# Kernel tuning notes

Hardware: AMD Instinct MI355X
Metric: run time of the kernel (lower is better)

## Reference

```python
import jax, jax.numpy as jnp
import numpy as np


def setup_inputs() -> dict:
    key = jax.random.key(0)
    ks = jax.random.split(key, 5)
    B, C, H, W = 8, 256, 64, 64
    Ck = C // 8  # 32, reduced channel dim
    return {
        "x": jax.random.normal(ks[0], (B, C, H, W), dtype=jnp.float32),
        "wf": jax.random.normal(ks[1], (Ck, C), dtype=jnp.float32) * 0.05,
        "wg": jax.random.normal(ks[2], (Ck, C), dtype=jnp.float32) * 0.05,
        "wh": jax.random.normal(ks[3], (Ck, C), dtype=jnp.float32) * 0.05,
        "wv": jax.random.normal(ks[4], (C, Ck), dtype=jnp.float32) * 0.05,
        "gamma": jnp.zeros((1,), dtype=jnp.float32),
    }


def reference(x, wf, wg, wh, wv, gamma):
    B, C, H, W = x.shape
    N = H * W
    xf = x.reshape(B, C, N)  # flatten spatial tokens
    # 1x1 convs == channel matmuls
    f = jnp.einsum('oc,bcn->bon', wf, xf)  # [B, Ck, N]
    g = jnp.einsum('oc,bcn->bon', wg, xf)  # [B, Ck, N]
    h = jnp.einsum('oc,bcn->bon', wh, xf)  # [B, Ck, N]
    # s = f^T @ g -> [B, N, N]; softmax over last axis (dim 2 in torch)
    s = jnp.einsum('bcn,bcm->bnm', f, g)
    beta = jax.nn.softmax(s, axis=2)
    # v = h @ beta  (note: beta NOT transposed, faithful to original)
    v = jnp.einsum('bcn,bnm->bcm', h, beta)  # [B, Ck, N]
    o = jnp.einsum('oc,bcm->bom', wv, v).reshape(B, C, H, W)
    return gamma * o + x
```

## Files before the change

kernel.cpp:

```cpp
#include <hip/hip_runtime.h>
#include <hip/hip_bf16.h>

#define BB 8
#define CC 256
#define CK 32
#define NN 4096

typedef short bf16x8 __attribute__((ext_vector_type(8)));
typedef float f32x4 __attribute__((ext_vector_type(4)));

#define MFMA(a, b, c) __builtin_amdgcn_mfma_f32_16x16x32_bf16((a), (b), (c), 0, 0, 0)

#define GLOAD16(gsrc, ldst) __builtin_amdgcn_global_load_lds( \
    (const __attribute__((address_space(1))) void*)(gsrc), \
    (__attribute__((address_space(3))) void*)(ldst), 16, 0, 0)

#define OBASE(b) ((size_t)(b) * 1048576)
#define OFF_F  0
#define OFF_G  65536
#define OFF_HT 131072
#define OFF_LE 196608
#define OFF_V0 200704
#define OFF_WB 786432
#define VSTRIDE 131072

#define SHIFT 24.0f

static __device__ __forceinline__ unsigned pack_trunc(float lo, float hi) {
  unsigned ulo = __builtin_bit_cast(unsigned, lo);
  unsigned uhi = __builtin_bit_cast(unsigned, hi);
  return (uhi & 0xFFFF0000u) | (ulo >> 16);
}
static __device__ __forceinline__ unsigned pack_rne(float lo, float hi) {
  unsigned ulo = __builtin_bit_cast(unsigned, lo);
  unsigned uhi = __builtin_bit_cast(unsigned, hi);
  ulo += 0x7FFFu + ((ulo >> 16) & 1u);
  uhi += 0x7FFFu + ((uhi >> 16) & 1u);
  return (uhi & 0xFFFF0000u) | (ulo >> 16);
}
static __device__ __forceinline__ unsigned short rne16(float v) {
  unsigned u = __builtin_bit_cast(unsigned, v);
  u += 0x7FFFu + ((u >> 16) & 1u);
  return (unsigned short)(u >> 16);
}

__global__ __launch_bounds__(256) void wcvt_kernel(
    const float* __restrict__ wf, const float* __restrict__ wg,
    const float* __restrict__ wh, float* __restrict__ sc)
{
  int w = blockIdx.x;
  int tid = threadIdx.x;
  const float* src = (w == 0) ? wf : ((w == 1) ? wg : wh);
  unsigned short* wb = (unsigned short*)(sc + OFF_WB) + w * 8192;
  for (int e = tid; e < 8192; e += 256) wb[e] = rne16(src[e]);
}

__global__ __launch_bounds__(256) void proj_kernel(
    const float* __restrict__ x, float* __restrict__ sc)
{
  __shared__ float t[64][69];
  __shared__ unsigned short tb[64][264];

  int tid = threadIdx.x, blk = blockIdx.x;
  int b = blk >> 6, n0 = (blk & 63) << 6;

  #pragma unroll 1
  for (int ct = 0; ct < 4; ++ct) {
    int c0 = ct << 6;
    const float* xb = x + ((size_t)b * CC + c0) * NN + n0;
    int ci0 = tid >> 4, j = (tid & 15) << 2;
    #pragma unroll
    for (int p = 0; p < 4; ++p) {
      int ci = p * 16 + ci0;
      float4 v = *(const float4*)&xb[(size_t)ci * NN + j];
      t[ci][j] = v.x; t[ci][j + 1] = v.y; t[ci][j + 2] = v.z; t[ci][j + 3] = v.w;
    }
    __syncthreads();
    int ni = tid >> 2, cq = (tid & 3) << 4;
    #pragma unroll
    for (int e = 0; e < 16; ++e)
      tb[ni][c0 + cq + e] = rne16(t[cq + e][ni]);
    __syncthreads();
  }

  int w = tid >> 6, lane = tid & 63, q = lane >> 4, c = lane & 15;
  int nb = n0 + (w << 4);
  const char* wB = (const char*)(sc + OFF_WB);
  const unsigned short* tbrow = &tb[(w << 4) + c][0];

  const f32x4 z4 = {0.f, 0.f, 0.f, 0.f};
  f32x4 fa0 = z4, fa1 = z4, ga0 = z4, ga1 = z4, ha0 = z4, ha1 = z4;

  #pragma unroll
  for (int kc = 0; kc < 8; ++kc) {
    int koe = kc * 32 + q * 8;
    int ko = kc * 64 + q * 16;
    bf16x8 xa = *(const bf16x8*)(tbrow + koe);
    bf16x8 w0 = *(const bf16x8*)(wB + (size_t)c * 512 + ko);
    bf16x8 w1 = *(const bf16x8*)(wB + (size_t)(16 + c) * 512 + ko);
    bf16x8 w2 = *(const bf16x8*)(wB + 16384 + (size_t)c * 512 + ko);
    bf16x8 w3 = *(const bf16x8*)(wB + 16384 + (size_t)(16 + c) * 512 + ko);
    bf16x8 w4 = *(const bf16x8*)(wB + 32768 + (size_t)c * 512 + ko);
    bf16x8 w5 = *(const bf16x8*)(wB + 32768 + (size_t)(16 + c) * 512 + ko);
    fa0 = MFMA(xa, w0, fa0);  fa1 = MFMA(xa, w1, fa1);
    ga0 = MFMA(xa, w2, ga0);  ga1 = MFMA(xa, w3, ga1);
    ha0 = MFMA(w4, xa, ha0);  ha1 = MFMA(w5, xa, ha1);
  }

  unsigned short* fD = (unsigned short*)(sc + OBASE(b) + OFF_F);
  unsigned short* gD = (unsigned short*)(sc + OBASE(b) + OFF_G);
  unsigned short* hD = (unsigned short*)(sc + OBASE(b) + OFF_HT);
  #pragma unroll
  for (int r = 0; r < 4; ++r) {
    int n = nb + q * 4 + r;
    fD[(size_t)n * 32 + c]      = rne16(fa0[r]);
    fD[(size_t)n * 32 + 16 + c] = rne16(fa1[r]);
    gD[(size_t)n * 32 + c]      = rne16(ga0[r]);
    gD[(size_t)n * 32 + 16 + c] = rne16(ga1[r]);
    hD[(size_t)(q * 4 + r) * NN + nb + c]        = rne16(ha0[r]);
    hD[(size_t)(16 + q * 4 + r) * NN + nb + c]   = rne16(ha1[r]);
  }
}

__global__ __launch_bounds__(256) void passb_kernel(float* __restrict__ sc)
{
  __shared__ float Zsh[2][16][4];
  int tid = threadIdx.x, blk = blockIdx.x;
  int b = blk >> 7, nb0 = (blk & 127) << 5;
  int w = tid >> 6, lane = tid & 63, q = lane >> 4, c = lane & 15;

  const char* fb = (const char*)(sc + OBASE(b) + OFF_F);
  const char* gb = (const char*)(sc + OBASE(b) + OFF_G);

  bf16x8 fa0 = *(const bf16x8*)(fb + (size_t)(nb0 + c) * 64 + q * 16);
  bf16x8 fa1 = *(const bf16x8*)(fb + (size_t)(nb0 + 16 + c) * 64 + q * 16);
  const f32x4 z4 = {0.f, 0.f, 0.f, 0.f};
  float za[2][4] = {{0.f,0.f,0.f,0.f},{0.f,0.f,0.f,0.f}};

  int mt0 = w << 10;
  bf16x8 g0 = *(const bf16x8*)(gb + (size_t)(mt0 + 0  + c) * 64 + q * 16);
  bf16x8 g1 = *(const bf16x8*)(gb + (size_t)(mt0 + 16 + c) * 64 + q * 16);
  bf16x8 g2 = *(const bf16x8*)(gb + (size_t)(mt0 + 32 + c) * 64 + q * 16);
  bf16x8 g3 = *(const bf16x8*)(gb + (size_t)(mt0 + 48 + c) * 64 + q * 16);

  for (int mt = mt0; mt < mt0 + 1024; mt += 64) {
    int mtn = (mt + 64 < mt0 + 1024) ? mt + 64 : mt0;
    bf16x8 n0 = *(const bf16x8*)(gb + (size_t)(mtn + 0  + c) * 64 + q * 16);
    bf16x8 n1 = *(const bf16x8*)(gb + (size_t)(mtn + 16 + c) * 64 + q * 16);
    bf16x8 n2 = *(const bf16x8*)(gb + (size_t)(mtn + 32 + c) * 64 + q * 16);
    bf16x8 n3 = *(const bf16x8*)(gb + (size_t)(mtn + 48 + c) * 64 + q * 16);
    f32x4 s;
    #define BSTEP(gk) \
      s = MFMA(fa0, gk, z4); \
      za[0][0] += __expf(s[0] - SHIFT); za[0][1] += __expf(s[1] - SHIFT); \
      za[0][2] += __expf(s[2] - SHIFT); za[0][3] += __expf(s[3] - SHIFT); \
      s = MFMA(fa1, gk, z4); \
      za[1][0] += __expf(s[0] - SHIFT); za[1][1] += __expf(s[1] - SHIFT); \
      za[1][2] += __expf(s[2] - SHIFT); za[1][3] += __expf(s[3] - SHIFT);
    BSTEP(g0) BSTEP(g1) BSTEP(g2) BSTEP(g3)
    #undef BSTEP
    g0 = n0; g1 = n1; g2 = n2; g3 = n3;
  }
  #pragma unroll
  for (int d = 1; d < 16; d <<= 1) {
    #pragma unroll
    for (int i = 0; i < 2; ++i)
      #pragma unroll
      for (int r = 0; r < 4; ++r) za[i][r] += __shfl_xor(za[i][r], d);
  }
  if (c == 0) {
    #pragma unroll
    for (int i = 0; i < 2; ++i)
      #pragma unroll
      for (int r = 0; r < 4; ++r) Zsh[i][q * 4 + r][w] = za[i][r];
  }
  __syncthreads();
  if (tid < 32) {
    int ns2 = tid >> 4, row = tid & 15;
    float Z = Zsh[ns2][row][0] + Zsh[ns2][row][1]
            + Zsh[ns2][row][2] + Zsh[ns2][row][3];
    sc[OBASE(b) + OFF_LE + nb0 + ns2 * 16 + row] = SHIFT + __logf(Z);
  }
}

__global__ __launch_bounds__(256, 4) void passc_kernel(float* __restrict__ sc)
{
  __shared__ unsigned Pt[128 * 32];
  __shared__ float Lsh[1024];
  __shared__ unsigned fsh[2][1024];
  __shared__ unsigned hsh[2][1024];

  int tid = threadIdx.x, blk = blockIdx.x;
  int b = blk >> 7, rest = blk & 127;
  int ns = rest & 3, mblk = rest >> 2;
  int m0 = mblk << 7;
  int nbase = ns << 10;
  int w = tid >> 6, lane = tid & 63, q = lane >> 4, c = lane & 15;
  int hc = tid >> 3, hslot = (tid & 7) ^ (hc & 7);

  const char* fb = (const char*)(sc + OBASE(b) + OFF_F);
  const char* gb = (const char*)(sc + OBASE(b) + OFF_G);
  const char* hb = (const char*)(sc + OBASE(b) + OFF_HT);
  const float* LE = sc + OBASE(b) + OFF_LE;

  for (int i = tid; i < 1024; i += 256) Lsh[i] = LE[nbase + i];

  bf16x8 gB0 = *(const bf16x8*)(gb + (size_t)(m0 + w * 16 + c) * 64 + q * 16);
  bf16x8 gB1 = *(const bf16x8*)(gb + (size_t)(m0 + 64 + w * 16 + c) * 64 + q * 16);

  GLOAD16(fb + (size_t)nbase * 64 + tid * 16, (char*)&fsh[0][0] + tid * 16);
  GLOAD16(hb + (size_t)hc * 8192 + (size_t)nbase * 2 + hslot * 16,
          (char*)&hsh[0][0] + tid * 16);
  __syncthreads();

  const f32x4 z4 = {0.f, 0.f, 0.f, 0.f};
  f32x4 v00 = z4, v01 = z4, v10 = z4, v11 = z4;

  unsigned sw = (unsigned)(c & 7) << 4;
  char* Pt0 = (char*)Pt + (size_t)(w * 16 + c) * 128;
  char* Pt1 = (char*)Pt + (size_t)(64 + w * 16 + c) * 128;

  int buf = 0;
  for (int nt = 0; nt < 1024; nt += 64) {
    if (nt + 64 < 1024) {
      GLOAD16(fb + (size_t)(nbase + nt + 64) * 64 + tid * 16,
              (char*)&fsh[buf ^ 1][0] + tid * 16);
      GLOAD16(hb + (size_t)hc * 8192 + (size_t)(nbase + nt + 64) * 2 + hslot * 16,
              (char*)&hsh[buf ^ 1][0] + tid * 16);
    }
    const char* fS = (const char*)&fsh[buf][0];
    const char* hS = (const char*)&hsh[buf][0];

    bf16x8 f0 = *(const bf16x8*)(fS + (0 * 16 + c) * 64 + q * 16);
    bf16x8 f1 = *(const bf16x8*)(fS + (1 * 16 + c) * 64 + q * 16);
    bf16x8 f2 = *(const bf16x8*)(fS + (2 * 16 + c) * 64 + q * 16);
    bf16x8 f3 = *(const bf16x8*)(fS + (3 * 16 + c) * 64 + q * 16);
    f32x4 sA0 = MFMA(f0, gB0, z4), sB0 = MFMA(f0, gB1, z4);
    f32x4 sA1 = MFMA(f1, gB0, z4), sB1 = MFMA(f1, gB1, z4);
    f32x4 sA2 = MFMA(f2, gB0, z4), sB2 = MFMA(f2, gB1, z4);
    f32x4 sA3 = MFMA(f3, gB0, z4), sB3 = MFMA(f3, gB1, z4);

    #pragma unroll
    for (int sub = 0; sub < 4; ++sub) {
      f32x4 sA = (sub == 0) ? sA0 : (sub == 1) ? sA1 : (sub == 2) ? sA2 : sA3;
      f32x4 sB = (sub == 0) ? sB0 : (sub == 1) ? sB1 : (sub == 2) ? sB2 : sB3;
      const f32x4 Lt = *(const f32x4*)&Lsh[nt + sub * 16 + q * 4];
      uint2 pkA, pkB;
      pkA.x = pack_trunc(__expf(sA[0] - Lt[0]), __expf(sA[1] - Lt[1]));
      pkA.y = pack_trunc(__expf(sA[2] - Lt[2]), __expf(sA[3] - Lt[3]));
      pkB.x = pack_trunc(__expf(sB[0] - Lt[0]), __expf(sB[1] - Lt[1]));
      pkB.y = pack_trunc(__expf(sB[2] - Lt[2]), __expf(sB[3] - Lt[3]));
      unsigned off = ((unsigned)(sub * 32 + q * 8)) ^ sw;
      *(uint2*)(Pt0 + off) = pkA;
      *(uint2*)(Pt1 + off) = pkB;
    }

    #pragma unroll
    for (int ks = 0; ks < 2; ++ks) {
      unsigned off = ((unsigned)(ks * 64 + q * 16)) ^ sw;
      bf16x8 pb0 = *(const bf16x8*)(Pt0 + off);
      bf16x8 pb1 = *(const bf16x8*)(Pt1 + off);
      bf16x8 h0 = *(const bf16x8*)(hS + c * 128 + off);
      bf16x8 h1 = *(const bf16x8*)(hS + (16 + c) * 128 + off);
      v00 = MFMA(h0, pb0, v00);
      v10 = MFMA(h1, pb0, v10);
      v01 = MFMA(h0, pb1, v01);
      v11 = MFMA(h1, pb1, v11);
    }
    __syncthreads();
    buf ^= 1;
  }

  float* V = sc + OBASE(b) + OFF_V0 + (size_t)ns * VSTRIDE;
  {
    int mA = m0 + w * 16 + c, mB = m0 + 64 + w * 16 + c;
    size_t bA = (size_t)(mA & 31) * 4096 + (size_t)(mA >> 5) * 32;
    size_t bB = (size_t)(mB & 31) * 4096 + (size_t)(mB >> 5) * 32;
    *(f32x4*)&V[bA + q * 4]      = v00;
    *(f32x4*)&V[bA + 16 + q * 4] = v10;
    *(f32x4*)&V[bB + q * 4]      = v01;
    *(f32x4*)&V[bB + 16 + q * 4] = v11;
  }
}

__global__ __launch_bounds__(256) void epi_kernel(
    float* out, const float* __restrict__ x,
    const float* __restrict__ wv, const float* __restrict__ gamma)
{
  int tid = threadIdx.x, blk = blockIdx.x;
  int b = blk >> 7;
  int m0 = (blk & 127) << 5;
  int w = tid >> 6, lane = tid & 63, q = lane >> 4, c = lane & 15;
  int co0 = w << 6;

  const float* V0 = out + OBASE(b) + OFF_V0;

  bf16x8 Bf[2];
  #pragma unroll
  for (int mt = 0; mt < 2; ++mt) {
    int ml = mt * 16 + c;
    size_t base = (size_t)ml * 4096 + (size_t)(m0 >> 5) * 32 + q * 8;
    float4 a0 = {0,0,0,0}, a1 = {0,0,0,0};
    #pragma unroll
    for (int i = 0; i < 4; ++i) {
      const float* Vi = V0 + (size_t)i * VSTRIDE;
      float4 p0 = *(const float4*)&Vi[base];
      float4 p1 = *(const float4*)&Vi[base + 4];
      a0.x += p0.x; a0.y += p0.y; a0.z += p0.z; a0.w += p0.w;
      a1.x += p1.x; a1.y += p1.y; a1.z += p1.z; a1.w += p1.w;
    }
    unsigned u0 = pack_rne(a0.x, a0.y);
    unsigned u1 = pack_rne(a0.z, a0.w);
    unsigned u2 = pack_rne(a1.x, a1.y);
    unsigned u3 = pack_rne(a1.z, a1.w);
    Bf[mt] = __builtin_bit_cast(bf16x8, make_uint4(u0, u1, u2, u3));
  }
  bf16x8 Af[4];
  #pragma unroll
  for (int ci = 0; ci < 4; ++ci) {
    const float* wr = wv + (size_t)(co0 + ci * 16 + c) * 32 + q * 8;
    float4 a0 = *(const float4*)wr;
    float4 a1 = *(const float4*)(wr + 4);
    unsigned u0 = pack_rne(a0.x, a0.y);
    unsigned u1 = pack_rne(a0.z, a0.w);
    unsigned u2 = pack_rne(a1.x, a1.y);
    unsigned u3 = pack_rne(a1.z, a1.w);
    Af[ci] = __builtin_bit_cast(bf16x8, make_uint4(u0, u1, u2, u3));
  }
  __syncthreads();

  const f32x4 z4 = {0.f, 0.f, 0.f, 0.f};
  const float g0 = gamma[0];
  #pragma unroll
  for (int ci = 0; ci < 4; ++ci) {
    #pragma unroll
    for (int mt = 0; mt < 2; ++mt) {
      f32x4 acc = MFMA(Af[ci], Bf[mt], z4);
      #pragma unroll
      for (int r = 0; r < 4; ++r) {
        int co = co0 + ci * 16 + q * 4 + r;
        size_t idx = ((size_t)b * CC + co) * NN + m0 + mt * 16 + c;
        out[idx] = g0 * acc[r] + x[idx];
      }
    }
  }
}

extern "C" void kernel_launch(void* const* d_in, const int* in_sizes, int n_in,
                              void* d_out, int out_size, void* d_ws, size_t ws_size,
                              hipStream_t stream) {
  const float* x     = (const float*)d_in[0];
  const float* wf    = (const float*)d_in[1];
  const float* wg    = (const float*)d_in[2];
  const float* wh    = (const float*)d_in[3];
  const float* wv    = (const float*)d_in[4];
  const float* gamma = (const float*)d_in[5];
  float* out = (float*)d_out;

  wcvt_kernel <<<3,    256, 0, stream>>>(wf, wg, wh, out);
  proj_kernel <<<512,  256, 0, stream>>>(x, out);
  passb_kernel<<<1024, 256, 0, stream>>>(out);
  passc_kernel<<<1024, 256, 0, stream>>>(out);
  epi_kernel  <<<1024, 256, 0, stream>>>(out, x, wv, gamma);
}
```

Baseline: 108.8 us.

## Fold softmax normalizer into h, use exp2 with constant shift, vectorize epilogue

Passb now computes the reciprocal of each row's softmax sum and scales the corresponding h columns in place, instead of storing a per-row log-sum. Passc can then use a fixed shift with exp2 and a fused multiply-add rather than loading and subtracting per-row normalizers, which removes the shared-memory normalizer load. The epilogue stages MFMA results through shared memory so that x is read and out written as coalesced float4 rows. The trade-off is an extra h rounding step, an in-place read-modify-write in passb, and the LDS transpose in the epilogue.

```diff
diff --git a/kernel.cpp b/kernel.cpp
--- a/kernel.cpp
+++ b/kernel.cpp
@@ -19,12 +19,13 @@
 #define OFF_F  0
 #define OFF_G  65536
 #define OFF_HT 131072
-#define OFF_LE 196608
 #define OFF_V0 200704
 #define OFF_WB 786432
 #define VSTRIDE 131072
 
 #define SHIFT 24.0f
+#define L2E 1.44269504089f
+#define S2  34.6246810188f
 
 static __device__ __forceinline__ unsigned pack_trunc(float lo, float hi) {
   unsigned ulo = __builtin_bit_cast(unsigned, lo);
@@ -43,6 +44,7 @@
   u += 0x7FFFu + ((u >> 16) & 1u);
   return (unsigned short)(u >> 16);
 }
+static __device__ __forceinline__ float fexp2(float y) { return __builtin_exp2f(y); }
 
 __global__ __launch_bounds__(256) void wcvt_kernel(
     const float* __restrict__ wf, const float* __restrict__ wg,
@@ -125,6 +127,7 @@
 __global__ __launch_bounds__(256) void passb_kernel(float* __restrict__ sc)
 {
   __shared__ float Zsh[2][16][4];
+  __shared__ float Rsh[32];
   int tid = threadIdx.x, blk = blockIdx.x;
   int b = blk >> 7, nb0 = (blk & 127) << 5;
   int w = tid >> 6, lane = tid & 63, q = lane >> 4, c = lane & 15;
@@ -179,14 +182,28 @@
     int ns2 = tid >> 4, row = tid & 15;
     float Z = Zsh[ns2][row][0] + Zsh[ns2][row][1]
             + Zsh[ns2][row][2] + Zsh[ns2][row][3];
-    sc[OBASE(b) + OFF_LE + nb0 + ns2 * 16 + row] = SHIFT + __logf(Z);
+    Rsh[ns2 * 16 + row] = 1.0f / Z;
+  }
+  __syncthreads();
+  {
+    int cidx = tid >> 3, jj = (tid & 7) << 2;
+    unsigned short* hp = (unsigned short*)(sc + OBASE(b) + OFF_HT)
+                       + (size_t)cidx * NN + nb0 + jj;
+    uint2 hv = *(const uint2*)hp;
+    float h0 = __builtin_bit_cast(float, hv.x << 16)          * Rsh[jj + 0];
+    float h1 = __builtin_bit_cast(float, hv.x & 0xFFFF0000u)  * Rsh[jj + 1];
+    float h2 = __builtin_bit_cast(float, hv.y << 16)          * Rsh[jj + 2];
+    float h3 = __builtin_bit_cast(float, hv.y & 0xFFFF0000u)  * Rsh[jj + 3];
+    uint2 ov;
+    ov.x = pack_rne(h0, h1);
+    ov.y = pack_rne(h2, h3);
+    *(uint2*)hp = ov;
   }
 }
 
 __global__ __launch_bounds__(256, 4) void passc_kernel(float* __restrict__ sc)
 {
-  __shared__ unsigned Pt[128 * 32];
-  __shared__ float Lsh[1024];
+  __shared__ unsigned Pt[128 * 32 + 1024];
   __shared__ unsigned fsh[2][1024];
   __shared__ unsigned hsh[2][1024];
 
@@ -201,9 +218,6 @@
   const char* fb = (const char*)(sc + OBASE(b) + OFF_F);
   const char* gb = (const char*)(sc + OBASE(b) + OFF_G);
   const char* hb = (const char*)(sc + OBASE(b) + OFF_HT);
-  const float* LE = sc + OBASE(b) + OFF_LE;
-
-  for (int i = tid; i < 1024; i += 256) Lsh[i] = LE[nbase + i];
 
   bf16x8 gB0 = *(const bf16x8*)(gb + (size_t)(m0 + w * 16 + c) * 64 + q * 16);
   bf16x8 gB1 = *(const bf16x8*)(gb + (size_t)(m0 + 64 + w * 16 + c) * 64 + q * 16);
@@ -244,12 +258,11 @@
     for (int sub = 0; sub < 4; ++sub) {
       f32x4 sA = (sub == 0) ? sA0 : (sub == 1) ? sA1 : (sub == 2) ? sA2 : sA3;
       f32x4 sB = (sub == 0) ? sB0 : (sub == 1) ? sB1 : (sub == 2) ? sB2 : sB3;
-      const f32x4 Lt = *(const f32x4*)&Lsh[nt + sub * 16 + q * 4];
       uint2 pkA, pkB;
-      pkA.x = pack_trunc(__expf(sA[0] - Lt[0]), __expf(sA[1] - Lt[1]));
-      pkA.y = pack_trunc(__expf(sA[2] - Lt[2]), __expf(sA[3] - Lt[3]));
-      pkB.x = pack_trunc(__expf(sB[0] - Lt[0]), __expf(sB[1] - Lt[1]));
-      pkB.y = pack_trunc(__expf(sB[2] - Lt[2]), __expf(sB[3] - Lt[3]));
+      pkA.x = pack_trunc(fexp2(fmaf(sA[0], L2E, -S2)), fexp2(fmaf(sA[1], L2E, -S2)));
+      pkA.y = pack_trunc(fexp2(fmaf(sA[2], L2E, -S2)), fexp2(fmaf(sA[3], L2E, -S2)));
+      pkB.x = pack_trunc(fexp2(fmaf(sB[0], L2E, -S2)), fexp2(fmaf(sB[1], L2E, -S2)));
+      pkB.y = pack_trunc(fexp2(fmaf(sB[2], L2E, -S2)), fexp2(fmaf(sB[3], L2E, -S2)));
       unsigned off = ((unsigned)(sub * 32 + q * 8)) ^ sw;
       *(uint2*)(Pt0 + off) = pkA;
       *(uint2*)(Pt1 + off) = pkB;
@@ -287,6 +300,7 @@
     float* out, const float* __restrict__ x,
     const float* __restrict__ wv, const float* __restrict__ gamma)
 {
+  __shared__ float vt[256][36];
   int tid = threadIdx.x, blk = blockIdx.x;
   int b = blk >> 7;
   int m0 = (blk & 127) << 5;
@@ -327,22 +341,34 @@
     unsigned u3 = pack_rne(a1.z, a1.w);
     Af[ci] = __builtin_bit_cast(bf16x8, make_uint4(u0, u1, u2, u3));
   }
-  __syncthreads();
 
   const f32x4 z4 = {0.f, 0.f, 0.f, 0.f};
-  const float g0 = gamma[0];
   #pragma unroll
   for (int ci = 0; ci < 4; ++ci) {
     #pragma unroll
     for (int mt = 0; mt < 2; ++mt) {
       f32x4 acc = MFMA(Af[ci], Bf[mt], z4);
       #pragma unroll
-      for (int r = 0; r < 4; ++r) {
-        int co = co0 + ci * 16 + q * 4 + r;
-        size_t idx = ((size_t)b * CC + co) * NN + m0 + mt * 16 + c;
-        out[idx] = g0 * acc[r] + x[idx];
-      }
-    }
+      for (int r = 0; r < 4; ++r)
+        vt[co0 + ci * 16 + q * 4 + r][mt * 16 + c] = acc[r];
+    }
+  }
+  __syncthreads();
+
+  const float g0 = gamma[0];
+  int rsub = lane >> 3, col = (lane & 7) << 2;
+  #pragma unroll
+  for (int p = 0; p < 8; ++p) {
+    int row = (w << 6) + (p << 3) + rsub;
+    f32x4 v = *(const f32x4*)&vt[row][col];
+    size_t idx = ((size_t)b * CC + row) * NN + m0 + col;
+    float4 xv = *(const float4*)&x[idx];
+    float4 o;
+    o.x = g0 * v[0] + xv.x;
+    o.y = g0 * v[1] + xv.y;
+    o.z = g0 * v[2] + xv.z;
+    o.w = g0 * v[3] + xv.w;
+    *(float4*)&out[idx] = o;
   }
 }
 
```

After: 119.2 us. +9.5%, slower.
